# Kernel tuning notes

Hardware: AMD Instinct MI355X
Metric: run time of the kernel (lower is better)

## Reference

```python
import jax, jax.numpy as jnp
import numpy as np

N, IN_DIM, OUT_DIM, HEADS = 50000, 128, 32, 8
E = 800000
F = OUT_DIM * HEADS  # 256 fused output features
SEM_HID = 128        # SemanticAttention hidden size (HAN default)


def setup_inputs() -> dict:
    key = jax.random.key(0)
    ks = jax.random.split(key, 16)
    inp = {
        "h": jax.random.normal(ks[0], (N, IN_DIM), jnp.float32),
        "src_a": jax.random.randint(ks[1], (E,), 0, N, jnp.int32),
        "dst_a": jax.random.randint(ks[2], (E,), 0, N, jnp.int32),
        "src_b": jax.random.randint(ks[3], (E,), 0, N, jnp.int32),
        "dst_b": jax.random.randint(ks[4], (E,), 0, N, jnp.int32),
    }
    s = 1.0 / np.sqrt(IN_DIM)
    # per-metapath GATConv params
    inp["W_a"] = jax.random.normal(ks[5], (IN_DIM, F), jnp.float32) * s
    inp["al_a"] = jax.random.normal(ks[6], (HEADS, OUT_DIM), jnp.float32) * 0.1
    inp["ar_a"] = jax.random.normal(ks[7], (HEADS, OUT_DIM), jnp.float32) * 0.1
    inp["bias_a"] = jnp.zeros((F,), jnp.float32)
    inp["W_b"] = jax.random.normal(ks[8], (IN_DIM, F), jnp.float32) * s
    inp["al_b"] = jax.random.normal(ks[9], (HEADS, OUT_DIM), jnp.float32) * 0.1
    inp["ar_b"] = jax.random.normal(ks[10], (HEADS, OUT_DIM), jnp.float32) * 0.1
    inp["bias_b"] = jnp.zeros((F,), jnp.float32)
    # semantic attention params
    inp["Wsem"] = jax.random.normal(ks[11], (F, SEM_HID), jnp.float32) / np.sqrt(F)
    inp["bsem"] = jnp.zeros((SEM_HID,), jnp.float32)
    inp["wsem"] = jax.random.normal(ks[12], (SEM_HID,), jnp.float32) / np.sqrt(SEM_HID)
    return inp


def gat_conv(h, src, dst, W, al, ar, bias):
    # h: [N, in_dim] -> feat: [N, H, D]
    feat = (h @ W).reshape(N, HEADS, OUT_DIM)
    el = (feat * al).sum(-1)  # [N, H]
    er = (feat * ar).sum(-1)  # [N, H]
    e = jax.nn.leaky_relu(el[src] + er[dst], 0.2)  # [E, H]
    # edge softmax over incoming edges of each dst node (numerically stable)
    m = jax.ops.segment_max(e, dst, num_segments=N)        # -inf for empty
    ex = jnp.exp(e - m[dst])                               # [E, H]
    denom = jax.ops.segment_sum(ex, dst, num_segments=N)   # [N, H]
    msg = feat[src] * ex[:, :, None]                       # [E, H, D]
    out = jax.ops.segment_sum(msg, dst, num_segments=N)    # [N, H, D]
    out = out / jnp.where(denom > 0, denom, 1.0)[:, :, None]
    return jax.nn.elu(out.reshape(N, F) + bias)


def reference(h, src_a, dst_a, src_b, dst_b,
              W_a, al_a, ar_a, bias_a,
              W_b, al_b, ar_b, bias_b,
              Wsem, bsem, wsem):
    z_a = gat_conv(h, src_a, dst_a, W_a, al_a, ar_a, bias_a)
    z_b = gat_conv(h, src_b, dst_b, W_b, al_b, ar_b, bias_b)
    z = jnp.stack([z_a, z_b], axis=1)                 # [N, M, F]
    q = jnp.tanh(z @ Wsem + bsem) @ wsem              # [N, M]
    beta = jax.nn.softmax(q.mean(axis=0))             # [M]
    return (z * beta[None, :, None]).sum(axis=1)      # [N, F]
```

## Files before the change

### kernel.cpp

```cpp
#include <hip/hip_runtime.h>
#include <stdint.h>

#define NN 50000
#define EE 800000
#define IN_DIM 128
#define OUT_DIM 32
#define HEADS 8
#define FF 256
#define SH 128
#define NPAD 50048
#define FEXT 272
#define CAP 64
#define CSTRIDE 16

#define GEMM_BLKS 782
#define FILL_G   6250
#define PULL_G   12500

#define P_BTA0   128
#define P_BTB0   (P_BTA0 + FEXT)
#define P_G      (P_BTB0 + FEXT)

#define F_GEMM   (2 * GEMM_BLKS)
#define F_G      (F_GEMM + FILL_G)

#define C_G      (2 * PULL_G)
#define D_G      (2 * GEMM_BLKS)

typedef short s16x8 __attribute__((ext_vector_type(8)));
typedef float f32x4 __attribute__((ext_vector_type(4)));
typedef float f32x2 __attribute__((ext_vector_type(2)));

__device__ __forceinline__ float b2f(unsigned short u) {
    union { unsigned int i; float f; } v; v.i = ((unsigned int)u) << 16; return v.f;
}
__device__ __forceinline__ unsigned short f2b(float f) {
    union { float f; unsigned int i; } v; v.f = f;
    unsigned int i = v.i;
    unsigned int r = (i + 0x7FFFu + ((i >> 16) & 1u)) >> 16;
    return (unsigned short)r;
}

__device__ __forceinline__ void buildBT_one(
    const float* __restrict__ W, const float* __restrict__ al,
    const float* __restrict__ ar, unsigned short* __restrict__ BT,
    int fp, int k)
{
    float v;
    if (fp < FF) {
        v = W[(size_t)k * FF + fp];
    } else if (fp < FF + 8) {
        int hh = fp - FF;
        float s = 0.f;
        #pragma unroll
        for (int d = 0; d < 32; ++d) s += W[(size_t)k * FF + hh * 32 + d] * al[hh * 32 + d];
        v = s;
    } else {
        int hh = fp - FF - 8;
        float s = 0.f;
        #pragma unroll
        for (int d = 0; d < 32; ++d) s += W[(size_t)k * FF + hh * 32 + d] * ar[hh * 32 + d];
        v = s;
    }
    BT[(size_t)fp * IN_DIM + k] = f2b(v);
}

__device__ __forceinline__ void dev_fill(
    int idx, const int* __restrict__ src, const int* __restrict__ dst,
    int* __restrict__ counts, unsigned short* __restrict__ perm)
{
    int d = dst[idx];
    int r = atomicAdd(&counts[d * CSTRIDE], 1);
    if (r < CAP) perm[d * CAP + r] = (unsigned short)src[idx];
}

__device__ __forceinline__ void dev_gemm(
    int gb, int t, const float* __restrict__ h,
    const unsigned short* __restrict__ BT,
    unsigned short* __restrict__ feat,
    float* __restrict__ el, float* __restrict__ er)
{
    int wave = t >> 6, lane = t & 63;
    int quad = lane >> 4, l16 = lane & 15;
    int nbase = gb * 64 + wave * 16;
    int n = nbase + l16;
    int nr = (n < NN) ? n : (NN - 1);
    const float* hrow = h + (size_t)nr * IN_DIM + quad * 8;
    s16x8 nfr[4];
    #pragma unroll
    for (int kt = 0; kt < 4; ++kt) {
        float4 p0 = *(const float4*)(hrow + kt * 32);
        float4 p1 = *(const float4*)(hrow + kt * 32 + 4);
        s16x8 v;
        v[0] = (short)f2b(p0.x); v[1] = (short)f2b(p0.y);
        v[2] = (short)f2b(p0.z); v[3] = (short)f2b(p0.w);
        v[4] = (short)f2b(p1.x); v[5] = (short)f2b(p1.y);
        v[6] = (short)f2b(p1.z); v[7] = (short)f2b(p1.w);
        nfr[kt] = v;
    }
    bool live = (n < NN);
    #pragma unroll 1
    for (int ft = 0; ft < 17; ++ft) {
        const unsigned short* brow = BT + (size_t)(ft * 16 + l16) * IN_DIM + quad * 8;
        f32x4 c = {0.f, 0.f, 0.f, 0.f};
        #pragma unroll
        for (int kt = 0; kt < 4; ++kt) {
            s16x8 ffr = *(const s16x8*)(brow + kt * 32);
            c = __builtin_amdgcn_mfma_f32_16x16x32_bf16(ffr, nfr[kt], c, 0, 0, 0);
        }
        if (ft < 16) {
            if (live) {
                ushort4 r;
                r.x = f2b(c[0]); r.y = f2b(c[1]); r.z = f2b(c[2]); r.w = f2b(c[3]);
                *(ushort4*)(feat + (size_t)n * FF + ft * 16 + quad * 4) = r;
            }
        } else if (live) {
            #pragma unroll
            for (int r = 0; r < 4; ++r) {
                int jp = quad * 4 + r;
                if (jp < 8) el[n * HEADS + jp] = c[r];
                else        er[n * HEADS + (jp - 8)] = c[r];
            }
        }
    }
}

__device__ __forceinline__ void dev_pull(
    int blk, int tid,
    const int* __restrict__ counts, const unsigned short* __restrict__ perm,
    const float* __restrict__ el, const float* __restrict__ er,
    const unsigned short* __restrict__ feat, const float* __restrict__ bias,
    unsigned short* __restrict__ zb)
{
    int wave = tid >> 6;
    int lane = tid & 63;
    int n = blk * 4 + wave;
    int sub = lane >> 5;
    int l32 = lane & 31;
    int head = l32 >> 2;
    int fbase = l32 * 8;
    int deg = counts[n * CSTRIDE];
    if (deg > CAP) deg = CAP;
    int base = n * CAP;
    float ern = er[n * HEADS + head];
    float den = 0.f;
    f32x2 acc2[4];
    #pragma unroll
    for (int u = 0; u < 4; ++u) { acc2[u][0] = 0.f; acc2[u][1] = 0.f; }

#define PROC(EV, FV) {                                               \
        float x = (EV) + ern;                                        \
        x = fmaxf(x, 0.2f * x);                                      \
        float ex = __expf(x);                                        \
        den += ex;                                                   \
        f32x2 ex2; ex2[0] = ex; ex2[1] = ex;                         \
        const unsigned int* fp = (const unsigned int*)&(FV);         \
        _Pragma("unroll")                                            \
        for (int u = 0; u < 4; ++u) {                                \
            union { unsigned int i; float f; } lo, hi;               \
            lo.i = fp[u] << 16; hi.i = fp[u] & 0xFFFF0000u;          \
            f32x2 v; v[0] = lo.f; v[1] = hi.f;                       \
            acc2[u] += v * ex2;                                      \
        } }

    int jp = sub;
    #pragma unroll 1
    for (; jp + 6 < deg; jp += 8) {
        int s0 = perm[base + jp];
        int s1 = perm[base + jp + 2];
        int s2 = perm[base + jp + 4];
        int s3 = perm[base + jp + 6];
        float e0 = el[s0 * HEADS + head];
        float e1 = el[s1 * HEADS + head];
        float e2 = el[s2 * HEADS + head];
        float e3 = el[s3 * HEADS + head];
        uint4 f0 = *(const uint4*)(feat + (size_t)s0 * FF + fbase);
        uint4 f1 = *(const uint4*)(feat + (size_t)s1 * FF + fbase);
        uint4 f2 = *(const uint4*)(feat + (size_t)s2 * FF + fbase);
        uint4 f3 = *(const uint4*)(feat + (size_t)s3 * FF + fbase);
        PROC(e0, f0); PROC(e1, f1); PROC(e2, f2); PROC(e3, f3);
    }
    #pragma unroll 1
    for (; jp + 2 < deg; jp += 4) {
        int s0 = perm[base + jp];
        int s1 = perm[base + jp + 2];
        float e0 = el[s0 * HEADS + head];
        float e1 = el[s1 * HEADS + head];
        uint4 f0 = *(const uint4*)(feat + (size_t)s0 * FF + fbase);
        uint4 f1 = *(const uint4*)(feat + (size_t)s1 * FF + fbase);
        PROC(e0, f0); PROC(e1, f1);
    }
    if (jp < deg) {
        int s0 = perm[base + jp];
        float e0 = el[s0 * HEADS + head];
        uint4 f0 = *(const uint4*)(feat + (size_t)s0 * FF + fbase);
        PROC(e0, f0);
    }
#undef PROC

    float accf[8];
    #pragma unroll
    for (int u = 0; u < 4; ++u) {
        accf[2 * u]     = acc2[u][0];
        accf[2 * u + 1] = acc2[u][1];
    }

    den += __shfl_xor(den, 32, 64);
    #pragma unroll
    for (int u = 0; u < 8; ++u) accf[u] += __shfl_xor(accf[u], 32, 64);

    if (den <= 0.f) den = 1.f;
    float inv = 1.f / den;
    float4 b0 = *(const float4*)(bias + fbase);
    float4 b1 = *(const float4*)(bias + fbase + 4);
    float bv[8] = {b0.x, b0.y, b0.z, b0.w, b1.x, b1.y, b1.z, b1.w};
    if (sub == 0) {
        ushort4 r0, r1;
        unsigned short rr[8];
        #pragma unroll
        for (int u = 0; u < 8; ++u) {
            float ov = accf[u] * inv + bv[u];
            ov = (ov > 0.f) ? ov : (__expf(ov) - 1.f);
            rr[u] = f2b(ov);
        }
        r0.x = rr[0]; r0.y = rr[1]; r0.z = rr[2]; r0.w = rr[3];
        r1.x = rr[4]; r1.y = rr[5]; r1.z = rr[6]; r1.w = rr[7];
        *(ushort4*)(zb + (size_t)n * FF + fbase) = r0;
        *(ushort4*)(zb + (size_t)n * FF + fbase + 4) = r1;
    }
}

__global__ __launch_bounds__(256) void prep(
    const float* __restrict__ Wsem, unsigned short* __restrict__ WsemT,
    const float* __restrict__ W_a, const float* __restrict__ al_a,
    const float* __restrict__ ar_a, unsigned short* __restrict__ BT_a,
    const float* __restrict__ W_b, const float* __restrict__ al_b,
    const float* __restrict__ ar_b, unsigned short* __restrict__ BT_b)
{
    int b = blockIdx.x, t = threadIdx.x;
    if (b < P_BTA0) {
        WsemT[b * FF + t] = f2b(Wsem[(size_t)t * SH + b]);
    } else if (b < P_BTB0) {
        if (t < IN_DIM) buildBT_one(W_a, al_a, ar_a, BT_a, b - P_BTA0, t);
    } else {
        if (t < IN_DIM) buildBT_one(W_b, al_b, ar_b, BT_b, b - P_BTB0, t);
    }
}

__global__ __launch_bounds__(256) void megaF(
    const float* __restrict__ h,
    const unsigned short* __restrict__ BT_a, const unsigned short* __restrict__ BT_b,
    unsigned short* __restrict__ feat_a, unsigned short* __restrict__ feat_b,
    float* __restrict__ el_a, float* __restrict__ er_a,
    float* __restrict__ el_b, float* __restrict__ er_b,
    const int* __restrict__ src_a, const int* __restrict__ dst_a,
    const int* __restrict__ src_b, const int* __restrict__ dst_b,
    int* __restrict__ counts_a, int* __restrict__ counts_b,
    unsigned short* __restrict__ perm_a, unsigned short* __restrict__ perm_b)
{
    int b = blockIdx.x, t = threadIdx.x;
    if (b >= F_GEMM) {
        int idx = (b - F_GEMM) * 256 + t;
        if (idx < EE) dev_fill(idx, src_a, dst_a, counts_a, perm_a);
        else          dev_fill(idx - EE, src_b, dst_b, counts_b, perm_b);
        return;
    }
    int mp = (b >= GEMM_BLKS);
    int gb = mp ? b - GEMM_BLKS : b;
    dev_gemm(gb, t, h,
             mp ? BT_b : BT_a, mp ? feat_b : feat_a,
             mp ? el_b : el_a, mp ? er_b : er_a);
}

__global__ __launch_bounds__(256, 8) void megaC(
    const int* __restrict__ counts_a, const int* __restrict__ counts_b,
    const unsigned short* __restrict__ perm_a, const unsigned short* __restrict__ perm_b,
    const float* __restrict__ el_a, const float* __restrict__ er_a,
    const float* __restrict__ el_b, const float* __restrict__ er_b,
    const unsigned short* __restrict__ feat_a, const unsigned short* __restrict__ feat_b,
    const float* __restrict__ bias_a, const float* __restrict__ bias_b,
    unsigned short* __restrict__ zb_a, unsigned short* __restrict__ zb_b)
{
    int bb = blockIdx.x;
    int mp = (bb >= PULL_G);
    int blk = mp ? bb - PULL_G : bb;
    dev_pull(blk, threadIdx.x,
             mp ? counts_b : counts_a, mp ? perm_b : perm_a,
             mp ? el_b : el_a, mp ? er_b : er_a,
             mp ? feat_b : feat_a, mp ? bias_b : bias_a,
             mp ? zb_b : zb_a);
}

__global__ __launch_bounds__(256) void megaD(
    const unsigned short* __restrict__ zb_a, const unsigned short* __restrict__ zb_b,
    const unsigned short* __restrict__ WsemT,
    const float* __restrict__ bsem, const float* __restrict__ wsem,
    float* __restrict__ qsum)
{
    __shared__ unsigned short wlds[SH * FF];
    int bb = blockIdx.x;
    int mp = (bb >= GEMM_BLKS);
    int blk = mp ? bb - GEMM_BLKS : bb;
    const unsigned short* zb = mp ? zb_b : zb_a;

    #pragma unroll
    for (int i = 0; i < 16; ++i) {
        int off = threadIdx.x * 8 + i * 2048;
        *(s16x8*)&wlds[off] = *(const s16x8*)&WsemT[off];
    }
    __syncthreads();

    int wave = threadIdx.x >> 6, lane = threadIdx.x & 63;
    int quad = lane >> 4, l16 = lane & 15;
    int nbase = blk * 64 + wave * 16;
    const unsigned short* arow = zb + (size_t)(nbase + l16) * FF + quad * 8;
    s16x8 afr[8];
    #pragma unroll
    for (int kt = 0; kt < 8; ++kt)
        afr[kt] = *(const s16x8*)(arow + kt * 32);
    float qacc = 0.f;
    #pragma unroll 2
    for (int jt = 0; jt < 8; ++jt) {
        int jj = jt * 16 + l16;
        const unsigned short* brow = &wlds[jj * FF + quad * 8];
        f32x4 c = {0.f, 0.f, 0.f, 0.f};
        #pragma unroll
        for (int kt = 0; kt < 8; ++kt) {
            s16x8 bfr = *(const s16x8*)(brow + kt * 32);
            c = __builtin_amdgcn_mfma_f32_16x16x32_bf16(afr[kt], bfr, c, 0, 0, 0);
        }
        float bj = bsem[jj], wj = wsem[jj];
        #pragma unroll
        for (int r = 0; r < 4; ++r) {
            int n = nbase + quad * 4 + r;
            float y = c[r] + bj;
            y = fminf(fmaxf(y, -10.f), 10.f);
            float t = __expf(2.f * y);
            float tv = (t - 1.f) * __builtin_amdgcn_rcpf(t + 1.f) * wj;
            qacc += (n < NN) ? tv : 0.f;
        }
    }
    #pragma unroll
    for (int o = 1; o < 64; o <<= 1) qacc += __shfl_xor(qacc, o, 64);
    if (lane == 0) atomicAdd(&qsum[mp], qacc);
}

__global__ __launch_bounds__(256) void combine_kernel(
    const unsigned short* __restrict__ za,
    const unsigned short* __restrict__ zbm,
    float* __restrict__ out, const float* __restrict__ qsum)
{
    size_t i = (size_t)blockIdx.x * blockDim.x + threadIdx.x;
    size_t base = i * 8;
    if (base >= (size_t)NN * FF) return;
    float qa = qsum[0] * (1.f / NN), qb = qsum[1] * (1.f / NN);
    float mx = fmaxf(qa, qb);
    float ea = __expf(qa - mx), eb = __expf(qb - mx);
    float inv = 1.f / (ea + eb);
    float b0 = ea * inv, b1 = eb * inv;
    uint4 va = *(const uint4*)(za + base);
    uint4 vb = *(const uint4*)(zbm + base);
    const unsigned short* pa = (const unsigned short*)&va;
    const unsigned short* pb = (const unsigned short*)&vb;
    float4 r0, r1;
    r0.x = b0 * b2f(pa[0]) + b1 * b2f(pb[0]);
    r0.y = b0 * b2f(pa[1]) + b1 * b2f(pb[1]);
    r0.z = b0 * b2f(pa[2]) + b1 * b2f(pb[2]);
    r0.w = b0 * b2f(pa[3]) + b1 * b2f(pb[3]);
    r1.x = b0 * b2f(pa[4]) + b1 * b2f(pb[4]);
    r1.y = b0 * b2f(pa[5]) + b1 * b2f(pb[5]);
    r1.z = b0 * b2f(pa[6]) + b1 * b2f(pb[6]);
    r1.w = b0 * b2f(pa[7]) + b1 * b2f(pb[7]);
    *(float4*)(out + base) = r0;
    *(float4*)(out + base + 4) = r1;
}

extern "C" void kernel_launch(void* const* d_in, const int* in_sizes, int n_in,
                              void* d_out, int out_size, void* d_ws, size_t ws_size,
                              hipStream_t stream)
{
    const float* h      = (const float*)d_in[0];
    const int* src_a    = (const int*)d_in[1];
    const int* dst_a    = (const int*)d_in[2];
    const int* src_b    = (const int*)d_in[3];
    const int* dst_b    = (const int*)d_in[4];
    const float* W_a    = (const float*)d_in[5];
    const float* al_a   = (const float*)d_in[6];
    const float* ar_a   = (const float*)d_in[7];
    const float* bias_a = (const float*)d_in[8];
    const float* W_b    = (const float*)d_in[9];
    const float* al_b   = (const float*)d_in[10];
    const float* ar_b   = (const float*)d_in[11];
    const float* bias_b = (const float*)d_in[12];
    const float* Wsem   = (const float*)d_in[13];
    const float* bsem   = (const float*)d_in[14];
    const float* wsem   = (const float*)d_in[15];
    float* out = (float*)d_out;

    char* ws = (char*)d_ws;
    size_t o = 0;
    auto alloc = [&](size_t bytes) -> char* {
        char* p = ws + o;
        o += (bytes + 255) & ~(size_t)255;
        return p;
    };
    unsigned short* BT_a   = (unsigned short*)alloc((size_t)FEXT * IN_DIM * 2);
    unsigned short* BT_b   = (unsigned short*)alloc((size_t)FEXT * IN_DIM * 2);
    unsigned short* feat_a = (unsigned short*)alloc((size_t)NN * FF * 2);
    unsigned short* feat_b = (unsigned short*)alloc((size_t)NN * FF * 2);
    unsigned short* zb_a   = (unsigned short*)alloc((size_t)NPAD * FF * 2);
    unsigned short* zb_b   = (unsigned short*)alloc((size_t)NPAD * FF * 2);
    unsigned short* WsemT  = (unsigned short*)alloc((size_t)SH * FF * 2);
    float* el_a    = (float*)alloc((size_t)NN * HEADS * 4);
    float* er_a    = (float*)alloc((size_t)NN * HEADS * 4);
    float* el_b    = (float*)alloc((size_t)NN * HEADS * 4);
    float* er_b    = (float*)alloc((size_t)NN * HEADS * 4);
    unsigned short* perm_a = (unsigned short*)alloc((size_t)NN * CAP * 2);
    unsigned short* perm_b = (unsigned short*)alloc((size_t)NN * CAP * 2);
    char* zspan0   = ws + o;
    int* counts_a  = (int*)alloc((size_t)NN * CSTRIDE * 4);
    int* counts_b  = (int*)alloc((size_t)NN * CSTRIDE * 4);
    float* qsum    = (float*)alloc(8);
    size_t zspan   = (size_t)((ws + o) - zspan0);

    hipMemsetAsync(zspan0, 0, zspan, stream);
    prep<<<P_G, 256, 0, stream>>>(Wsem, WsemT,
                                  W_a, al_a, ar_a, BT_a,
                                  W_b, al_b, ar_b, BT_b);
    megaF<<<F_G, 256, 0, stream>>>(h, BT_a, BT_b, feat_a, feat_b,
                                   el_a, er_a, el_b, er_b,
                                   src_a, dst_a, src_b, dst_b,
                                   counts_a, counts_b, perm_a, perm_b);
    megaC<<<C_G, 256, 0, stream>>>(counts_a, counts_b, perm_a, perm_b,
                                   el_a, er_a, el_b, er_b,
                                   feat_a, feat_b, bias_a, bias_b, zb_a, zb_b);
    megaD<<<D_G, 256, 0, stream>>>(zb_a, zb_b, WsemT, bsem, wsem, qsum);
    combine_kernel<<<(int)(((size_t)NN * FF / 8 + 255) / 256), 256, 0, stream>>>(zb_a, zb_b, out, qsum);
}
```

Before: 488.6 us.

## Fuse semantic-attention projection into edge-softmax pull kernel via per-wave LDS MFMA

Removes the separate megaD kernel. Each wave now keeps its finished bf16 z row in LDS and immediately runs the Wsem projection, tanh and wsem dot product with MFMA. WsemT is read straight from global memory per wave. This avoids re-reading the full z arrays and one kernel launch, but it wastes MFMA work because all 16 A rows are the same node, and it pushes a lot of cached traffic through each wave's WsemT reads. The q accumulation is spread over 16 padded slots per metapath to reduce atomic contention, and combine_kernel sums those slots.

```diff
diff --git a/kernel.cpp b/kernel.cpp
--- a/kernel.cpp
+++ b/kernel.cpp
@@ -25,7 +25,8 @@
 #define F_G      (F_GEMM + FILL_G)
 
 #define C_G      (2 * PULL_G)
-#define D_G      (2 * GEMM_BLKS)
+
+#define QSLOTS   16
 
 typedef short s16x8 __attribute__((ext_vector_type(8)));
 typedef float f32x4 __attribute__((ext_vector_type(4)));
@@ -125,15 +126,74 @@
     }
 }
 
-__device__ __forceinline__ void dev_pull(
-    int blk, int tid,
-    const int* __restrict__ counts, const unsigned short* __restrict__ perm,
-    const float* __restrict__ el, const float* __restrict__ er,
-    const unsigned short* __restrict__ feat, const float* __restrict__ bias,
-    unsigned short* __restrict__ zb)
-{
-    int wave = tid >> 6;
-    int lane = tid & 63;
+__global__ __launch_bounds__(256) void prep(
+    const float* __restrict__ Wsem, unsigned short* __restrict__ WsemT,
+    const float* __restrict__ W_a, const float* __restrict__ al_a,
+    const float* __restrict__ ar_a, unsigned short* __restrict__ BT_a,
+    const float* __restrict__ W_b, const float* __restrict__ al_b,
+    const float* __restrict__ ar_b, unsigned short* __restrict__ BT_b)
+{
+    int b = blockIdx.x, t = threadIdx.x;
+    if (b < P_BTA0) {
+        WsemT[b * FF + t] = f2b(Wsem[(size_t)t * SH + b]);
+    } else if (b < P_BTB0) {
+        if (t < IN_DIM) buildBT_one(W_a, al_a, ar_a, BT_a, b - P_BTA0, t);
+    } else {
+        if (t < IN_DIM) buildBT_one(W_b, al_b, ar_b, BT_b, b - P_BTB0, t);
+    }
+}
+
+__global__ __launch_bounds__(256) void megaF(
+    const float* __restrict__ h,
+    const unsigned short* __restrict__ BT_a, const unsigned short* __restrict__ BT_b,
+    unsigned short* __restrict__ feat_a, unsigned short* __restrict__ feat_b,
+    float* __restrict__ el_a, float* __restrict__ er_a,
+    float* __restrict__ el_b, float* __restrict__ er_b,
+    const int* __restrict__ src_a, const int* __restrict__ dst_a,
+    const int* __restrict__ src_b, const int* __restrict__ dst_b,
+    int* __restrict__ counts_a, int* __restrict__ counts_b,
+    unsigned short* __restrict__ perm_a, unsigned short* __restrict__ perm_b)
+{
+    int b = blockIdx.x, t = threadIdx.x;
+    if (b >= F_GEMM) {
+        int idx = (b - F_GEMM) * 256 + t;
+        if (idx < EE) dev_fill(idx, src_a, dst_a, counts_a, perm_a);
+        else          dev_fill(idx - EE, src_b, dst_b, counts_b, perm_b);
+        return;
+    }
+    int mp = (b >= GEMM_BLKS);
+    int gb = mp ? b - GEMM_BLKS : b;
+    dev_gemm(gb, t, h,
+             mp ? BT_b : BT_a, mp ? feat_b : feat_a,
+             mp ? el_b : el_a, mp ? er_b : er_a);
+}
+
+__global__ __launch_bounds__(256, 8) void megaC(
+    const int* __restrict__ counts_a, const int* __restrict__ counts_b,
+    const unsigned short* __restrict__ perm_a, const unsigned short* __restrict__ perm_b,
+    const float* __restrict__ el_a, const float* __restrict__ er_a,
+    const float* __restrict__ el_b, const float* __restrict__ er_b,
+    const unsigned short* __restrict__ feat_a, const unsigned short* __restrict__ feat_b,
+    const float* __restrict__ bias_a, const float* __restrict__ bias_b,
+    unsigned short* __restrict__ zb_a, unsigned short* __restrict__ zb_b,
+    const unsigned short* __restrict__ WsemT,
+    const float* __restrict__ bsem, const float* __restrict__ wsem,
+    float* __restrict__ qsumP)
+{
+    __shared__ __align__(16) unsigned short zlds[4][256];
+    int bb = blockIdx.x;
+    int mp = (bb >= PULL_G);
+    int blk = mp ? bb - PULL_G : bb;
+    const int* counts = mp ? counts_b : counts_a;
+    const unsigned short* perm = mp ? perm_b : perm_a;
+    const float* el = mp ? el_b : el_a;
+    const float* er = mp ? er_b : er_a;
+    const unsigned short* feat = mp ? feat_b : feat_a;
+    const float* bias = mp ? bias_b : bias_a;
+    unsigned short* zb = mp ? zb_b : zb_a;
+
+    int wave = threadIdx.x >> 6;
+    int lane = threadIdx.x & 63;
     int n = blk * 4 + wave;
     int sub = lane >> 5;
     int l32 = lane & 31;
@@ -214,146 +274,72 @@
     float4 b0 = *(const float4*)(bias + fbase);
     float4 b1 = *(const float4*)(bias + fbase + 4);
     float bv[8] = {b0.x, b0.y, b0.z, b0.w, b1.x, b1.y, b1.z, b1.w};
+
+    unsigned short rr[8];
+    #pragma unroll
+    for (int u = 0; u < 8; ++u) {
+        float ov = accf[u] * inv + bv[u];
+        ov = (ov > 0.f) ? ov : (__expf(ov) - 1.f);
+        rr[u] = f2b(ov);
+    }
     if (sub == 0) {
         ushort4 r0, r1;
-        unsigned short rr[8];
-        #pragma unroll
-        for (int u = 0; u < 8; ++u) {
-            float ov = accf[u] * inv + bv[u];
-            ov = (ov > 0.f) ? ov : (__expf(ov) - 1.f);
-            rr[u] = f2b(ov);
-        }
         r0.x = rr[0]; r0.y = rr[1]; r0.z = rr[2]; r0.w = rr[3];
         r1.x = rr[4]; r1.y = rr[5]; r1.z = rr[6]; r1.w = rr[7];
         *(ushort4*)(zb + (size_t)n * FF + fbase) = r0;
         *(ushort4*)(zb + (size_t)n * FF + fbase + 4) = r1;
-    }
-}
-
-__global__ __launch_bounds__(256) void prep(
-    const float* __restrict__ Wsem, unsigned short* __restrict__ WsemT,
-    const float* __restrict__ W_a, const float* __restrict__ al_a,
-    const float* __restrict__ ar_a, unsigned short* __restrict__ BT_a,
-    const float* __restrict__ W_b, const float* __restrict__ al_b,
-    const float* __restrict__ ar_b, unsigned short* __restrict__ BT_b)
-{
-    int b = blockIdx.x, t = threadIdx.x;
-    if (b < P_BTA0) {
-        WsemT[b * FF + t] = f2b(Wsem[(size_t)t * SH + b]);
-    } else if (b < P_BTB0) {
-        if (t < IN_DIM) buildBT_one(W_a, al_a, ar_a, BT_a, b - P_BTA0, t);
-    } else {
-        if (t < IN_DIM) buildBT_one(W_b, al_b, ar_b, BT_b, b - P_BTB0, t);
-    }
-}
-
-__global__ __launch_bounds__(256) void megaF(
-    const float* __restrict__ h,
-    const unsigned short* __restrict__ BT_a, const unsigned short* __restrict__ BT_b,
-    unsigned short* __restrict__ feat_a, unsigned short* __restrict__ feat_b,
-    float* __restrict__ el_a, float* __restrict__ er_a,
-    float* __restrict__ el_b, float* __restrict__ er_b,
-    const int* __restrict__ src_a, const int* __restrict__ dst_a,
-    const int* __restrict__ src_b, const int* __restrict__ dst_b,
-    int* __restrict__ counts_a, int* __restrict__ counts_b,
-    unsigned short* __restrict__ perm_a, unsigned short* __restrict__ perm_b)
-{
-    int b = blockIdx.x, t = threadIdx.x;
-    if (b >= F_GEMM) {
-        int idx = (b - F_GEMM) * 256 + t;
-        if (idx < EE) dev_fill(idx, src_a, dst_a, counts_a, perm_a);
-        else          dev_fill(idx - EE, src_b, dst_b, counts_b, perm_b);
-        return;
-    }
-    int mp = (b >= GEMM_BLKS);
-    int gb = mp ? b - GEMM_BLKS : b;
-    dev_gemm(gb, t, h,
-             mp ? BT_b : BT_a, mp ? feat_b : feat_a,
-             mp ? el_b : el_a, mp ? er_b : er_a);
-}
-
-__global__ __launch_bounds__(256, 8) void megaC(
-    const int* __restrict__ counts_a, const int* __restrict__ counts_b,
-    const unsigned short* __restrict__ perm_a, const unsigned short* __restrict__ perm_b,
-    const float* __restrict__ el_a, const float* __restrict__ er_a,
-    const float* __restrict__ el_b, const float* __restrict__ er_b,
-    const unsigned short* __restrict__ feat_a, const unsigned short* __restrict__ feat_b,
-    const float* __restrict__ bias_a, const float* __restrict__ bias_b,
-    unsigned short* __restrict__ zb_a, unsigned short* __restrict__ zb_b)
-{
-    int bb = blockIdx.x;
-    int mp = (bb >= PULL_G);
-    int blk = mp ? bb - PULL_G : bb;
-    dev_pull(blk, threadIdx.x,
-             mp ? counts_b : counts_a, mp ? perm_b : perm_a,
-             mp ? el_b : el_a, mp ? er_b : er_a,
-             mp ? feat_b : feat_a, mp ? bias_b : bias_a,
-             mp ? zb_b : zb_a);
-}
-
-__global__ __launch_bounds__(256) void megaD(
-    const unsigned short* __restrict__ zb_a, const unsigned short* __restrict__ zb_b,
-    const unsigned short* __restrict__ WsemT,
-    const float* __restrict__ bsem, const float* __restrict__ wsem,
-    float* __restrict__ qsum)
-{
-    __shared__ unsigned short wlds[SH * FF];
-    int bb = blockIdx.x;
-    int mp = (bb >= GEMM_BLKS);
-    int blk = mp ? bb - GEMM_BLKS : bb;
-    const unsigned short* zb = mp ? zb_b : zb_a;
-
-    #pragma unroll
-    for (int i = 0; i < 16; ++i) {
-        int off = threadIdx.x * 8 + i * 2048;
-        *(s16x8*)&wlds[off] = *(const s16x8*)&WsemT[off];
-    }
-    __syncthreads();
-
-    int wave = threadIdx.x >> 6, lane = threadIdx.x & 63;
-    int quad = lane >> 4, l16 = lane & 15;
-    int nbase = blk * 64 + wave * 16;
-    const unsigned short* arow = zb + (size_t)(nbase + l16) * FF + quad * 8;
-    s16x8 afr[8];
-    #pragma unroll
-    for (int kt = 0; kt < 8; ++kt)
-        afr[kt] = *(const s16x8*)(arow + kt * 32);
-    float qacc = 0.f;
-    #pragma unroll 2
+        s16x8 zv;
+        #pragma unroll
+        for (int u = 0; u < 8; ++u) zv[u] = (short)rr[u];
+        *(s16x8*)&zlds[wave][fbase] = zv;
+    }
+    asm volatile("s_waitcnt lgkmcnt(0)" ::: "memory");
+    __builtin_amdgcn_sched_barrier(0);
+
+    int quad = lane >> 4, col = lane & 15;
+    s16x8 af[8];
+    #pragma unroll
+    for (int kk = 0; kk < 8; ++kk)
+        af[kk] = *(const s16x8*)&zlds[wave][kk * 32 + quad * 8];
+    float qpart = 0.f;
+    #pragma unroll 1
     for (int jt = 0; jt < 8; ++jt) {
-        int jj = jt * 16 + l16;
-        const unsigned short* brow = &wlds[jj * FF + quad * 8];
+        int j = jt * 16 + col;
+        const unsigned short* brow = WsemT + (size_t)j * FF + quad * 8;
         f32x4 c = {0.f, 0.f, 0.f, 0.f};
         #pragma unroll
-        for (int kt = 0; kt < 8; ++kt) {
-            s16x8 bfr = *(const s16x8*)(brow + kt * 32);
-            c = __builtin_amdgcn_mfma_f32_16x16x32_bf16(afr[kt], bfr, c, 0, 0, 0);
+        for (int kk = 0; kk < 8; ++kk) {
+            s16x8 bf = *(const s16x8*)(brow + kk * 32);
+            c = __builtin_amdgcn_mfma_f32_16x16x32_bf16(af[kk], bf, c, 0, 0, 0);
         }
-        float bj = bsem[jj], wj = wsem[jj];
-        #pragma unroll
-        for (int r = 0; r < 4; ++r) {
-            int n = nbase + quad * 4 + r;
-            float y = c[r] + bj;
-            y = fminf(fmaxf(y, -10.f), 10.f);
-            float t = __expf(2.f * y);
-            float tv = (t - 1.f) * __builtin_amdgcn_rcpf(t + 1.f) * wj;
-            qacc += (n < NN) ? tv : 0.f;
-        }
-    }
-    #pragma unroll
-    for (int o = 1; o < 64; o <<= 1) qacc += __shfl_xor(qacc, o, 64);
-    if (lane == 0) atomicAdd(&qsum[mp], qacc);
+        float y = c[0] + bsem[j];
+        y = fminf(fmaxf(y, -10.f), 10.f);
+        float t = __expf(2.f * y);
+        qpart += (t - 1.f) * __builtin_amdgcn_rcpf(t + 1.f) * wsem[j];
+    }
+    qpart += __shfl_xor(qpart, 1, 64);
+    qpart += __shfl_xor(qpart, 2, 64);
+    qpart += __shfl_xor(qpart, 4, 64);
+    qpart += __shfl_xor(qpart, 8, 64);
+    if (lane == 0)
+        atomicAdd(&qsumP[(mp * QSLOTS + (blk & (QSLOTS - 1))) * 16], qpart);
 }
 
 __global__ __launch_bounds__(256) void combine_kernel(
     const unsigned short* __restrict__ za,
     const unsigned short* __restrict__ zbm,
-    float* __restrict__ out, const float* __restrict__ qsum)
+    float* __restrict__ out, const float* __restrict__ qsumP)
 {
     size_t i = (size_t)blockIdx.x * blockDim.x + threadIdx.x;
     size_t base = i * 8;
     if (base >= (size_t)NN * FF) return;
-    float qa = qsum[0] * (1.f / NN), qb = qsum[1] * (1.f / NN);
+    float qa = 0.f, qb = 0.f;
+    #pragma unroll
+    for (int s = 0; s < QSLOTS; ++s) {
+        qa += qsumP[s * 16];
+        qb += qsumP[(QSLOTS + s) * 16];
+    }
+    qa *= (1.f / NN); qb *= (1.f / NN);
     float mx = fmaxf(qa, qb);
     float ea = __expf(qa - mx), eb = __expf(qb - mx);
     float inv = 1.f / (ea + eb);
@@ -420,7 +406,7 @@
     char* zspan0   = ws + o;
     int* counts_a  = (int*)alloc((size_t)NN * CSTRIDE * 4);
     int* counts_b  = (int*)alloc((size_t)NN * CSTRIDE * 4);
-    float* qsum    = (float*)alloc(8);
+    float* qsumP   = (float*)alloc((size_t)2 * QSLOTS * 16 * 4);
     size_t zspan   = (size_t)((ws + o) - zspan0);
 
     hipMemsetAsync(zspan0, 0, zspan, stream);
@@ -433,7 +419,7 @@
                                    counts_a, counts_b, perm_a, perm_b);
     megaC<<<C_G, 256, 0, stream>>>(counts_a, counts_b, perm_a, perm_b,
                                    el_a, er_a, el_b, er_b,
-                                   feat_a, feat_b, bias_a, bias_b, zb_a, zb_b);
-    megaD<<<D_G, 256, 0, stream>>>(zb_a, zb_b, WsemT, bsem, wsem, qsum);
-    combine_kernel<<<(int)(((size_t)NN * FF / 8 + 255) / 256), 256, 0, stream>>>(zb_a, zb_b, out, qsum);
-}
+                                   feat_a, feat_b, bias_a, bias_b, zb_a, zb_b,
+                                   WsemT, bsem, wsem, qsumP);
+    combine_kernel<<<(int)(((size_t)NN * FF / 8 + 255) / 256), 256, 0, stream>>>(zb_a, zb_b, out, qsumP);
+}
```

Measured after the change: 995.2 us. 2.04x slower.
